# Optimization experiments

Measured on AMD Instinct MI355X. Metric: run time of the kernel, lower is better.

The kernel has to match this reference:

```python
import jax, jax.numpy as jnp
import numpy as np

N_NODES = 50000
N_EDGES = 600000
D_EMB = 128
D_HID = 128
N_HEADS = 4
N_MABS = 7  # ISAB0(mab0,mab1), ISAB1(mab0,mab1), PMA, SAB, SAB
B, S = 16, 512
PROTO = 5


def setup_inputs() -> dict:
    key = jax.random.key(0)
    ks = jax.random.split(key, 24)
    nrm = lambda k, shape, s=0.05: jax.random.normal(k, shape, jnp.float32) * s
    node_embed = nrm(ks[0], (N_NODES + 1, D_EMB), 1.0).at[0].set(0.0)  # padding_idx=0
    return {
        'node_ids': jax.random.randint(ks[1], (B, S), 0, N_NODES),
        'edge_idx': jax.random.randint(ks[2], (2, N_EDGES), 0, N_NODES),
        'edge_attr': jax.random.normal(ks[3], (N_EDGES,), jnp.float32),
        'node_embed': node_embed,
        'lin_W': nrm(ks[4], (D_EMB, D_HID)), 'lin_b': jnp.zeros((D_HID,), jnp.float32),
        'gat_W': nrm(ks[5], (D_HID, D_HID)),
        'gat_att_src': nrm(ks[6], (D_HID,)), 'gat_att_dst': nrm(ks[7], (D_HID,)),
        'gat_bias': jnp.zeros((D_HID,), jnp.float32),
        'mab_Wq': nrm(ks[8], (N_MABS, D_HID, D_HID)), 'mab_bq': jnp.zeros((N_MABS, D_HID), jnp.float32),
        'mab_Wk': nrm(ks[9], (N_MABS, D_HID, D_HID)), 'mab_bk': jnp.zeros((N_MABS, D_HID), jnp.float32),
        'mab_Wv': nrm(ks[10], (N_MABS, D_HID, D_HID)), 'mab_bv': jnp.zeros((N_MABS, D_HID), jnp.float32),
        'mab_Wo': nrm(ks[11], (N_MABS, D_HID, D_HID)), 'mab_bo': jnp.zeros((N_MABS, D_HID), jnp.float32),
        'isab_I': nrm(ks[12], (2, 1, D_HID), 1.0),   # 2 ISAB blocks, num_inds=1
        'pma_S': nrm(ks[13], (1, D_HID), 1.0),       # num_outputs=1 seed
        'dec_W': nrm(ks[14], (D_HID, D_HID)), 'dec_b': jnp.zeros((D_HID,), jnp.float32),
        'prototypes': nrm(ks[15], (1, PROTO, D_HID), 1.0),
    }


def mab(Q, K, Wq, bq, Wk, bk, Wv, bv, Wo, bo):
    # Set-transformer MAB, ln=False; residual uses projected Q; scale by sqrt(full dim)
    D = Q.shape[-1]
    h, d = N_HEADS, D // N_HEADS
    Qp = Q @ Wq + bq
    Kp = K @ Wk + bk
    Vp = K @ Wv + bv
    sh = lambda x: x.reshape(x.shape[0], x.shape[1], h, d).transpose(0, 2, 1, 3)
    A = jax.nn.softmax(jnp.einsum('bhqd,bhkd->bhqk', sh(Qp), sh(Kp)) / np.sqrt(D).astype(np.float32))
    O = sh(Qp) + jnp.einsum('bhqk,bhkd->bhqd', A, sh(Vp))
    O = O.transpose(0, 2, 1, 3).reshape(Q.shape[0], Q.shape[1], D)
    return O + jax.nn.relu(O @ Wo + bo)


def reference(node_ids, edge_idx, edge_attr, node_embed, lin_W, lin_b, gat_W,
              gat_att_src, gat_att_dst, gat_bias, mab_Wq, mab_bq, mab_Wk, mab_bk,
              mab_Wv, mab_bv, mab_Wo, mab_bo, isab_I, pma_S, dec_W, dec_b, prototypes):
    # embed all nodes then linear
    x = node_embed[jnp.arange(N_NODES)] @ lin_W + lin_b          # [N, H]
    # GATConv (1 head, negative_slope=0.2, add_self_loops=True; edge_attr unused)
    loops = jnp.arange(N_NODES)
    src = jnp.concatenate([edge_idx[0], loops])
    dst = jnp.concatenate([edge_idx[1], loops])
    xw = x @ gat_W                                               # [N, H]
    a_s = xw @ gat_att_src                                       # [N]
    a_d = xw @ gat_att_dst
    e = jax.nn.leaky_relu(a_s[src] + a_d[dst], 0.2)              # [E+N]
    m = jax.ops.segment_max(e, dst, num_segments=N_NODES)
    ex = jnp.exp(e - m[dst])
    den = jax.ops.segment_sum(ex, dst, num_segments=N_NODES)
    coef = ex / den[dst]
    x = jax.ops.segment_sum(coef[:, None] * xw[src], dst, num_segments=N_NODES) + gat_bias
    # gather per-sample node sets
    X = x[node_ids]                                              # [B, S, H]
    b = X.shape[0]
    def mb(i, Q, K):
        return mab(Q, K, mab_Wq[i], mab_bq[i], mab_Wk[i], mab_bk[i],
                   mab_Wv[i], mab_bv[i], mab_Wo[i], mab_bo[i])
    # encoder: 2 ISAB blocks (num_inds=1)
    for i in range(2):
        Hb = mb(2 * i, jnp.broadcast_to(isab_I[i][None], (b, 1, D_HID)), X)
        X = mb(2 * i + 1, X, Hb)
    # decoder: PMA -> SAB -> SAB -> Linear
    X = mb(4, jnp.broadcast_to(pma_S[None], (b, 1, D_HID)), X)
    X = mb(5, X, X)
    X = mb(6, X, X)
    X = X @ dec_W + dec_b                                        # [B, 1, H]
    proto = jnp.broadcast_to(prototypes, (b, PROTO, D_HID))
    return jnp.concatenate([X, proto], axis=1)                   # [B, 6, H]
```

## Files before the change

kernel.cpp:

```cpp
#include <hip/hip_runtime.h>
#include <math.h>

#define N_NODES 50000
#define N_EDGES 600000
#define BATCH 16
#define SEQ 512
#define NROWS (BATCH*SEQ)
#define N_ITEMS (N_EDGES + N_NODES)

#define OFF_X      0L
#define OFF_ACC    1048576L
#define OFF_X2     2097152L
#define OFF_WC     3245728L
#define OFF_BC     3262112L
#define OFF_QP     3262240L
#define OFF_WKH    3262624L
#define OFF_CKH    3264160L
#define OFF_VAS    3264176L
#define OFF_VAD    3264304L
#define OFF_BFIN   3264432L
#define OFF_CSD    3264560L
#define OFF_VPOD   3264564L
#define OFF_UP     3266612L
#define OFF_SP     3332148L
#define OFF_PWH    3332660L
#define OFF_PWL    3373620L
#define OFF_MASK   3414580L
#define OFF_DEG    (OFF_MASK + 50000L)
#define OFF_FILL   (OFF_DEG + 8192L)
#define OFF_CNT    (OFF_FILL + 8192L)
#define ZERO_BYTES ((50000L + 8192L + 8192L + 4L) * 4L)
#define OFF_MAP    (OFF_CNT + 4L)
#define OFF_INV    (OFF_MAP + 50000L)
#define OFF_ROWPTR (OFF_INV + 8192L)
#define OFF_COL    (OFF_ROWPTR + 8194L)

typedef __attribute__((ext_vector_type(8))) short bf16x8;
typedef __attribute__((ext_vector_type(4))) float f32x4;
#define MFMA16(a,b,c) __builtin_amdgcn_mfma_f32_16x16x32_bf16(a,b,c,0,0,0)

__device__ __forceinline__ unsigned short f2bf_rne(float f) {
    unsigned int u = __float_as_uint(f);
    unsigned int r = u + 0x7FFFu + ((u >> 16) & 1u);
    return (unsigned short)(r >> 16);
}
__device__ __forceinline__ float bf2f(unsigned short h) {
    return __uint_as_float(((unsigned int)h) << 16);
}
__device__ __forceinline__ float wave_allsum(float x) {
    #pragma unroll
    for (int off = 32; off > 0; off >>= 1) x += __shfl_xor(x, off);
    return x;
}

__global__ __launch_bounds__(256) void prep_kernel(
    const float* __restrict__ lin_W, const float* __restrict__ lin_b,
    const float* __restrict__ gat_W,
    const float* __restrict__ mab_Wq, const float* __restrict__ mab_bq,
    const float* __restrict__ isab_I, const float* __restrict__ pma_S,
    float* __restrict__ Wc, float* __restrict__ bc, float* __restrict__ qp)
{
    int t = blockIdx.x * 256 + threadIdx.x;
    if (t < 16384) {
        int i = t >> 7, j = t & 127;
        float s = 0.f;
        for (int k = 0; k < 128; ++k) s += lin_W[i*128 + k] * gat_W[k*128 + j];
        Wc[t] = s;
    } else if (t < 16512) {
        int j = t - 16384;
        float s = 0.f;
        for (int k = 0; k < 128; ++k) s += lin_b[k] * gat_W[k*128 + j];
        bc[j] = s;
    } else if (t < 16896) {
        int u = t - 16512;
        int m = u >> 7, c = u & 127;
        int mi = m * 2;
        const float* vec = (m == 0) ? isab_I : (m == 1 ? isab_I + 128 : pma_S);
        float s = mab_bq[mi*128 + c];
        for (int k = 0; k < 128; ++k) s += vec[k] * mab_Wq[mi*16384 + k*128 + c];
        qp[u] = s;
    }
}

__global__ __launch_bounds__(256) void pack2_kernel(
    const float* __restrict__ Wc, const float* __restrict__ bc,
    const float* __restrict__ qp,
    const float* __restrict__ mab_Wq, const float* __restrict__ mab_Wo,
    const float* __restrict__ mab_Wk, const float* __restrict__ mab_bk,
    const float* __restrict__ att_src, const float* __restrict__ att_dst,
    const float* __restrict__ gat_bias, const int* __restrict__ node_ids,
    unsigned short* __restrict__ pWh, unsigned short* __restrict__ pWl,
    float* __restrict__ wkh, float* __restrict__ ckh,
    float* __restrict__ vas, float* __restrict__ vad,
    float* __restrict__ bfin, float* __restrict__ csd,
    int* __restrict__ mask)
{
    int b = blockIdx.x, t = threadIdx.x;
    if (b < 320) {
        int tid = b*256 + t;
        int m = tid >> 14;
        int e = tid & 16383;
        int j = e & 7, l = (e>>3) & 63, ct = (e>>9) & 7, kc = e >> 12;
        int k = kc*32 + (l>>4)*8 + j;
        int c = ct*16 + (l & 15);
        const float* src;
        if (m == 0) src = Wc;
        else if (m == 1) src = mab_Wq + 1*16384;
        else if (m == 2) src = mab_Wo + 1*16384;
        else if (m == 3) src = mab_Wq + 3*16384;
        else src = mab_Wo + 3*16384;
        float v = src[k*128 + c];
        unsigned short h = f2bf_rne(v);
        pWh[tid] = h;
        pWl[tid] = f2bf_rne(v - bf2f(h));
    } else if (b == 320) {
        for (int it = 0; it < 6; ++it) {
            int u = it*256 + t;
            int m = u >> 9, h = (u >> 7) & 3, j = u & 127;
            const float* Wk = mab_Wk + (2*m)*16384 + j*128 + h*32;
            const float* q  = qp + m*128 + h*32;
            float s = 0.f;
            #pragma unroll
            for (int d = 0; d < 32; ++d) s += Wk[d] * q[d];
            wkh[u] = s;
        }
        if (t < 12) {
            int m = t >> 2, h = t & 3;
            const float* bk = mab_bk + (2*m)*128 + h*32;
            const float* q  = qp + m*128 + h*32;
            float s = 0.f;
            #pragma unroll
            for (int d = 0; d < 32; ++d) s += bk[d] * q[d];
            ckh[t] = s;
        }
    } else if (b == 321) {
        if (t < 128) {
            float s = 0.f;
            for (int j = 0; j < 128; ++j) s += Wc[t*128 + j] * att_src[j];
            vas[t] = s;
            bfin[t] = bc[t] + gat_bias[t];
        } else {
            int k = t - 128;
            float s = 0.f;
            for (int j = 0; j < 128; ++j) s += Wc[k*128 + j] * att_dst[j];
            vad[k] = s;
        }
        if (t == 0) {
            float s = 0.f;
            for (int j = 0; j < 128; ++j) s += bc[j] * att_src[j];
            csd[0] = s;
        }
        if (t == 1) {
            float s = 0.f;
            for (int j = 0; j < 128; ++j) s += bc[j] * att_dst[j];
            csd[1] = s;
        }
    } else {
        int idx = (b - 322)*256 + t;
        mask[node_ids[idx]] = 1;
    }
}

__device__ __forceinline__ void mfma_stage(
    const float (*Xs)[132], int arow, int ao, int lane,
    const unsigned short* __restrict__ pWh, const unsigned short* __restrict__ pWl,
    f32x4 acc[8])
{
    #pragma unroll
    for (int kc = 0; kc < 4; ++kc) {
        float4 fa = *(const float4*)&Xs[arow][kc*32 + ao];
        float4 fb = *(const float4*)&Xs[arow][kc*32 + ao + 4];
        float f[8] = {fa.x, fa.y, fa.z, fa.w, fb.x, fb.y, fb.z, fb.w};
        bf16x8 ah, al;
        #pragma unroll
        for (int j = 0; j < 8; ++j) {
            unsigned short h = f2bf_rne(f[j]);
            ah[j] = (short)h;
            al[j] = (short)f2bf_rne(f[j] - bf2f(h));
        }
        #pragma unroll
        for (int ct = 0; ct < 8; ++ct) {
            int fo = ((kc*8 + ct)*64 + lane)*8;
            bf16x8 bh = *(const bf16x8*)(pWh + fo);
            bf16x8 bl = *(const bf16x8*)(pWl + fo);
            acc[ct] = MFMA16(ah, bh, acc[ct]);
            acc[ct] = MFMA16(ah, bl, acc[ct]);
            acc[ct] = MFMA16(al, bh, acc[ct]);
        }
    }
}

__device__ __forceinline__ void partA_phase(
    const float (*Xs)[132], const float (*wks)[128], float (*esm)[64],
    const float* __restrict__ ckh, int blk, int t,
    float* __restrict__ up, float* __restrict__ sp)
{
    const float scale = 0.088388347648318447f;
    int wv = t >> 6, lane = t & 63;
    {
        float l = 0.f;
        for (int d4 = 0; d4 < 128; d4 += 4) {
            float4 xv = *(const float4*)&Xs[lane][d4];
            l += xv.x*wks[wv][d4] + xv.y*wks[wv][d4+1]
               + xv.z*wks[wv][d4+2] + xv.w*wks[wv][d4+3];
        }
        float e = __expf((l + ckh[wv]) * scale);
        esm[wv][lane] = e;
        float s = e;
        #pragma unroll
        for (int off = 32; off > 0; off >>= 1) s += __shfl_down(s, off);
        if (lane == 0) sp[blk*4 + wv] = s;
    }
    __syncthreads();
    {
        int hh = t >> 7, d = t & 127;
        float a0 = 0.f, a1 = 0.f;
        for (int k = 0; k < 64; ++k) {
            float xv = Xs[k][d];
            a0 += esm[2*hh][k] * xv;
            a1 += esm[2*hh + 1][k] * xv;
        }
        up[(blk*4 + 2*hh)*128 + d] = a0;
        up[(blk*4 + 2*hh + 1)*128 + d] = a1;
    }
}

__global__ __launch_bounds__(256) void mfma_lin_kernel(
    const float* __restrict__ Xin,
    const unsigned short* __restrict__ pWh, const unsigned short* __restrict__ pWl,
    const float* __restrict__ b1, float* __restrict__ out)
{
    __shared__ float Xs[64][132];
    int t = threadIdx.x;
    long row0 = (long)blockIdx.x * 64;
    #pragma unroll
    for (int i = 0; i < 32; ++i) {
        int idx = i*256 + t;
        int r = idx >> 7, k = idx & 127;
        Xs[r][k] = Xin[(row0 + r)*128 + k];
    }
    __syncthreads();
    int lane = t & 63, wv = t >> 6;
    int arow = wv*16 + (lane & 15), ao = (lane >> 4)*8;
    int crow0 = wv*16 + (lane >> 4)*4, ccol = lane & 15;
    f32x4 acc[8];
    #pragma unroll
    for (int ct = 0; ct < 8; ++ct) { acc[ct][0]=0.f; acc[ct][1]=0.f; acc[ct][2]=0.f; acc[ct][3]=0.f; }
    mfma_stage(Xs, arow, ao, lane, pWh, pWl, acc);
    #pragma unroll
    for (int ct = 0; ct < 8; ++ct) {
        int cc = ct*16 + ccol;
        float bb = b1[cc];
        #pragma unroll
        for (int i = 0; i < 4; ++i)
            out[(row0 + crow0 + i)*128 + cc] = acc[ct][i] + bb;
    }
}

__global__ __launch_bounds__(256) void gatherA_kernel(
    const int* __restrict__ node_ids, const int* __restrict__ map,
    const float* __restrict__ X2, const float* __restrict__ wkh,
    const float* __restrict__ ckh,
    float* __restrict__ X, float* __restrict__ up, float* __restrict__ sp)
{
    __shared__ float Xs[64][132];
    __shared__ float wks[4][128];
    __shared__ float esm[4][64];
    __shared__ int cmap[64];
    int blk = blockIdx.x, t = threadIdx.x;
    long j0 = (long)blk * 64;
    if (t < 64) cmap[t] = map[node_ids[j0 + t]];
    #pragma unroll
    for (int i = 0; i < 2; ++i) { int u = i*256 + t; wks[u >> 7][u & 127] = wkh[u]; }
    __syncthreads();
    #pragma unroll
    for (int i = 0; i < 8; ++i) {
        int idx = i*256 + t;
        int r = idx >> 5, k4 = (idx & 31)*4;
        float4 v = *(const float4*)(X2 + (long)cmap[r]*128 + k4);
        *(float4*)&Xs[r][k4] = v;
        *(float4*)(X + (j0 + r)*128 + k4) = v;
    }
    __syncthreads();
    partA_phase(Xs, wks, esm, ckh, blk, t, up, sp);
}

__global__ __launch_bounds__(256) void odd_fused_kernel(
    const float* __restrict__ Xin,
    const unsigned short* __restrict__ pQh, const unsigned short* __restrict__ pQl,
    const float* __restrict__ bq, const float* __restrict__ vpod,
    const unsigned short* __restrict__ pOh, const unsigned short* __restrict__ pOl,
    const float* __restrict__ bo,
    const float* __restrict__ wkh, const float* __restrict__ ckh,
    float* __restrict__ Xout, float* __restrict__ up, float* __restrict__ sp)
{
    __shared__ float Xs[64][132];
    __shared__ float wks[4][128];
    __shared__ float esm[4][64];
    int blk = blockIdx.x, t = threadIdx.x;
    long row0 = (long)blk * 64;
    #pragma unroll
    for (int i = 0; i < 32; ++i) {
        int idx = i*256 + t;
        int r = idx >> 7, k = idx & 127;
        Xs[r][k] = Xin[(row0 + r)*128 + k];
    }
    #pragma unroll
    for (int i = 0; i < 2; ++i) { int u = i*256 + t; wks[u >> 7][u & 127] = wkh[u]; }
    __syncthreads();
    int lane = t & 63, wv = t >> 6;
    int arow = wv*16 + (lane & 15), ao = (lane >> 4)*8;
    int crow0 = wv*16 + (lane >> 4)*4, ccol = lane & 15;
    int bidx = (int)(row0 >> 9);
    f32x4 acc[8];
    #pragma unroll
    for (int ct = 0; ct < 8; ++ct) { acc[ct][0]=0.f; acc[ct][1]=0.f; acc[ct][2]=0.f; acc[ct][3]=0.f; }
    mfma_stage(Xs, arow, ao, lane, pQh, pQl, acc);
    #pragma unroll
    for (int ct = 0; ct < 8; ++ct) {
        int cc = ct*16 + ccol;
        float bb = bq[cc] + vpod[bidx*128 + cc];
        #pragma unroll
        for (int i = 0; i < 4; ++i) Xs[crow0 + i][cc] = acc[ct][i] + bb;
    }
    #pragma unroll
    for (int ct = 0; ct < 8; ++ct) { acc[ct][0]=0.f; acc[ct][1]=0.f; acc[ct][2]=0.f; acc[ct][3]=0.f; }
    mfma_stage(Xs, arow, ao, lane, pOh, pOl, acc);
    #pragma unroll
    for (int ct = 0; ct < 8; ++ct) {
        int cc = ct*16 + ccol;
        float bb = bo[cc];
        #pragma unroll
        for (int i = 0; i < 4; ++i) {
            float o1 = Xs[crow0 + i][cc];
            float v = o1 + fmaxf(acc[ct][i] + bb, 0.f);
            Xout[(row0 + crow0 + i)*128 + cc] = v;
            Xs[crow0 + i][cc] = v;
        }
    }
    __syncthreads();
    partA_phase(Xs, wks, esm, ckh, blk, t, up, sp);
}

__global__ __launch_bounds__(256) void assign_kernel(
    const int* __restrict__ mask, int* __restrict__ map,
    int* __restrict__ inv, int* __restrict__ counter)
{
    __shared__ int wbase[4];
    int i = blockIdx.x*256 + threadIdx.x;
    bool act = (i < N_NODES) && mask[i];
    unsigned long long m = __ballot(act);
    int lane = threadIdx.x & 63;
    int w = threadIdx.x >> 6;
    if (lane == 0) wbase[w] = __popcll(m);
    __syncthreads();
    if (threadIdx.x == 0) {
        int tot = wbase[0] + wbase[1] + wbase[2] + wbase[3];
        int base = atomicAdd(counter, tot);
        int r = base;
        #pragma unroll
        for (int j = 0; j < 4; ++j) { int cj = wbase[j]; wbase[j] = r; r += cj; }
    }
    __syncthreads();
    if (i < N_NODES) {
        int c = -1;
        if (act) {
            c = wbase[w] + __popcll(m & ((1ull << lane) - 1ull));
            inv[c] = i;
        }
        map[i] = c;
    }
}

__global__ __launch_bounds__(256) void pass1_kernel(
    const int* __restrict__ edge_idx, const int* __restrict__ map,
    int* __restrict__ deg)
{
    int i = blockIdx.x*256 + threadIdx.x;
    if (i >= N_ITEMS) return;
    int dd = (i < N_EDGES) ? edge_idx[N_EDGES + i] : i - N_EDGES;
    int c = map[dd];
    if (c >= 0) atomicAdd(&deg[c], 1);
}

__global__ __launch_bounds__(256) void scan_kernel(const int* __restrict__ deg,
                                                   int* __restrict__ rowptr)
{
    __shared__ int wsum[4];
    int t = threadIdx.x;
    int base = t * 32;
    int s = 0;
    #pragma unroll
    for (int j = 0; j < 32; ++j) s += deg[base + j];
    int lane = t & 63, w = t >> 6;
    int v = s;
    #pragma unroll
    for (int off = 1; off < 64; off <<= 1) {
        int n = __shfl_up(v, off);
        if (lane >= off) v += n;
    }
    if (lane == 63) wsum[w] = v;
    __syncthreads();
    int wo = 0;
    for (int i = 0; i < 4; ++i) if (i < w) wo += wsum[i];
    int run = wo + v - s;
    #pragma unroll
    for (int j = 0; j < 32; ++j) { rowptr[base + j] = run; run += deg[base + j]; }
    if (t == 255) rowptr[8192] = run;
}

__global__ __launch_bounds__(256) void pass2_kernel(
    const int* __restrict__ edge_idx, const int* __restrict__ map,
    const int* __restrict__ rowptr, int* __restrict__ fill,
    int* __restrict__ colx)
{
    int i = blockIdx.x*256 + threadIdx.x;
    if (i >= N_ITEMS) return;
    int s, dd;
    if (i < N_EDGES) { s = edge_idx[i]; dd = edge_idx[N_EDGES + i]; }
    else             { s = dd = i - N_EDGES; }
    int c = map[dd];
    if (c < 0) return;
    int pos = rowptr[c] + atomicAdd(&fill[c], 1);
    colx[pos] = s;
}

__global__ __launch_bounds__(256) void agg_kernel(
    const int* __restrict__ rowptr, const int* __restrict__ colx,
    const int* __restrict__ inv, const int* __restrict__ cnt,
    const float* __restrict__ vas, const float* __restrict__ vad,
    const float* __restrict__ csd,
    const float* __restrict__ embed, float* __restrict__ acc)
{
    int c = blockIdx.x*4 + (threadIdx.x >> 6);
    int lane = threadIdx.x & 63;
    if (c >= *cnt) return;
    float va0 = vas[2*lane], va1 = vas[2*lane + 1];
    float vb0 = vad[2*lane], vb1 = vad[2*lane + 1];
    float csd0 = csd[0], csd1 = csd[1];
    int dd = inv[c];
    float2 wrow = *(const float2*)(embed + (long)dd*128 + lane*2);
    float ad = wave_allsum(wrow.x*vb0 + wrow.y*vb1) + csd1;
    int beg = rowptr[c], end = rowptr[c + 1];
    float s0 = 0.f, s1 = 0.f, den = 0.f;
    for (int j = beg; j < end; ++j) {
        int s = colx[j];
        float2 v = *(const float2*)(embed + (long)s*128 + lane*2);
        float as = wave_allsum(v.x*va0 + v.y*va1) + csd0;
        float e = as + ad;
        e = (e > 0.f) ? e : 0.2f * e;
        float ex = __expf(e);
        den += ex;
        s0 += ex * v.x;
        s1 += ex * v.y;
    }
    float inv_d = 1.f / den;
    float* o = acc + (long)c*128 + lane*2;
    o[0] = s0 * inv_d;
    o[1] = s1 * inv_d;
}

__device__ __forceinline__ float matvec_qs(
    const float* __restrict__ W, const float* xs, float (*red)[128], int t)
{
    int c = t & 127, q = t >> 7;
    float acc = 0.f;
    #pragma unroll
    for (int j = 0; j < 32; ++j) {
        int k = q*32 + j;
        acc += xs[k] * W[k*128 + c];
    }
    red[q][c] = acc;
    __syncthreads();
    float s = 0.f;
    if (t < 128) s = red[0][t] + red[1][t] + red[2][t] + red[3][t];
    __syncthreads();
    return s;
}

__global__ __launch_bounds__(512) void attn_evenB_kernel(
    const float* __restrict__ up, const float* __restrict__ sp,
    const float* __restrict__ qp,
    const float* __restrict__ Wv, const float* __restrict__ bv,
    const float* __restrict__ Wo, const float* __restrict__ bo,
    const float* __restrict__ Wv1, const float* __restrict__ bv1,
    float* __restrict__ vpod)
{
    __shared__ float u_sm[4][128];
    __shared__ float red[4][128];
    __shared__ float qs[128], Ovec[128], Hsm[128];
    int b = blockIdx.x, t = threadIdx.x;
    {
        float s = Wv[t*32] + Wo[t*32] + Wv1[t*32];
        asm volatile("" :: "v"(s));
    }
    if (t < 128) qs[t] = qp[t];
    {
        int h = t >> 7, d = t & 127;
        float s = 0.f, dn = 0.f;
        #pragma unroll
        for (int c = 0; c < 8; ++c) {
            s  += up[((b*8 + c)*4 + h)*128 + d];
            dn += sp[(b*8 + c)*4 + h];
        }
        u_sm[h][d] = s / dn;
    }
    __syncthreads();
    {
        int q4 = t >> 7, c = t & 127, h = c >> 5;
        float a = 0.f;
        #pragma unroll
        for (int j = 0; j < 32; ++j) {
            int k = q4*32 + j;
            a += u_sm[h][k] * Wv[k*128 + c];
        }
        red[q4][c] = a;
    }
    __syncthreads();
    if (t < 128) Ovec[t] = qs[t] + red[0][t] + red[1][t] + red[2][t] + red[3][t] + bv[t];
    __syncthreads();
    float mv = matvec_qs(Wo, Ovec, red, t);
    if (t < 128) Hsm[t] = Ovec[t] + fmaxf(mv + bo[t], 0.f);
    __syncthreads();
    float mv2 = matvec_qs(Wv1, Hsm, red, t);
    if (t < 128) vpod[b*128 + t] = mv2 + bv1[t];
}

__global__ __launch_bounds__(512) void attn_pmaB_kernel(
    const float* __restrict__ up, const float* __restrict__ sp,
    const float* __restrict__ qp,
    const float* __restrict__ mab_Wq, const float* __restrict__ mab_bq,
    const float* __restrict__ mab_Wv, const float* __restrict__ mab_bv,
    const float* __restrict__ mab_Wo, const float* __restrict__ mab_bo,
    const float* __restrict__ dec_W, const float* __restrict__ dec_b,
    const float* __restrict__ protos, float* __restrict__ out)
{
    __shared__ float u_sm[4][128];
    __shared__ float red[4][128];
    __shared__ float qs[128], Ovec[128], S1[128], S2[128];
    int b = blockIdx.x, t = threadIdx.x;
    {
        const float* wq = mab_Wq + 5*16384;
        const float* wv = mab_Wv + 4*16384;
        const float* wo = mab_Wo + 4*16384;
        float s = 0.f;
        #pragma unroll
        for (int i = 0; i < 2; ++i) s += wq[(t + 512*i)*32];
        #pragma unroll
        for (int i = 0; i < 3; ++i) { s += wv[(t + 512*i)*32]; s += wo[(t + 512*i)*32]; }
        s += dec_W[t*32];
        asm volatile("" :: "v"(s));
    }
    if (t < 128) qs[t] = qp[t];
    {
        int h = t >> 7, d = t & 127;
        float s = 0.f, dn = 0.f;
        #pragma unroll
        for (int c = 0; c < 8; ++c) {
            s  += up[((b*8 + c)*4 + h)*128 + d];
            dn += sp[(b*8 + c)*4 + h];
        }
        u_sm[h][d] = s / dn;
    }
    __syncthreads();
    {
        int q4 = t >> 7, c = t & 127, h = c >> 5;
        float a = 0.f;
        #pragma unroll
        for (int j = 0; j < 32; ++j) {
            int k = q4*32 + j;
            a += u_sm[h][k] * (mab_Wv + 4*16384)[k*128 + c];
        }
        red[q4][c] = a;
    }
    __syncthreads();
    if (t < 128) Ovec[t] = qs[t] + red[0][t] + red[1][t] + red[2][t] + red[3][t]
                         + mab_bv[4*128 + t];
    __syncthreads();
    float mv = matvec_qs(mab_Wo + 4*16384, Ovec, red, t);
    if (t < 128) S1[t] = Ovec[t] + fmaxf(mv + mab_bo[4*128 + t], 0.f);
    __syncthreads();
    float q5 = matvec_qs(mab_Wq + 5*16384, S1, red, t);
    float v5 = matvec_qs(mab_Wv + 5*16384, S1, red, t);
    if (t < 128) S2[t] = q5 + mab_bq[5*128 + t] + v5 + mab_bv[5*128 + t];
    __syncthreads();
    float m5 = matvec_qs(mab_Wo + 5*16384, S2, red, t);
    if (t < 128) S1[t] = S2[t] + fmaxf(m5 + mab_bo[5*128 + t], 0.f);
    __syncthreads();
    float q6 = matvec_qs(mab_Wq + 6*16384, S1, red, t);
    float v6 = matvec_qs(mab_Wv + 6*16384, S1, red, t);
    if (t < 128) S2[t] = q6 + mab_bq[6*128 + t] + v6 + mab_bv[6*128 + t];
    __syncthreads();
    float m6 = matvec_qs(mab_Wo + 6*16384, S2, red, t);
    if (t < 128) S1[t] = S2[t] + fmaxf(m6 + mab_bo[6*128 + t], 0.f);
    __syncthreads();
    float y = matvec_qs(dec_W, S1, red, t);
    if (t < 128) out[b*768 + t] = y + dec_b[t];
    {
        int p = t >> 7, c = t & 127;
        out[b*768 + (1 + p)*128 + c] = protos[p*128 + c];
        if (t < 128) out[b*768 + 640 + t] = protos[512 + t];
    }
}

extern "C" void kernel_launch(void* const* d_in, const int* in_sizes, int n_in,
                              void* d_out, int out_size, void* d_ws, size_t ws_size,
                              hipStream_t stream)
{
    (void)in_sizes; (void)n_in; (void)out_size; (void)ws_size;
    const int*   node_ids  = (const int*)d_in[0];
    const int*   edge_idx  = (const int*)d_in[1];
    const float* node_embed= (const float*)d_in[3];
    const float* lin_W     = (const float*)d_in[4];
    const float* lin_b     = (const float*)d_in[5];
    const float* gat_W     = (const float*)d_in[6];
    const float* att_src   = (const float*)d_in[7];
    const float* att_dst   = (const float*)d_in[8];
    const float* gat_bias  = (const float*)d_in[9];
    const float* mab_Wq    = (const float*)d_in[10];
    const float* mab_bq    = (const float*)d_in[11];
    const float* mab_Wk    = (const float*)d_in[12];
    const float* mab_bk    = (const float*)d_in[13];
    const float* mab_Wv    = (const float*)d_in[14];
    const float* mab_bv    = (const float*)d_in[15];
    const float* mab_Wo    = (const float*)d_in[16];
    const float* mab_bo    = (const float*)d_in[17];
    const float* isab_I    = (const float*)d_in[18];
    const float* pma_S     = (const float*)d_in[19];
    const float* dec_W     = (const float*)d_in[20];
    const float* dec_b     = (const float*)d_in[21];
    const float* protos    = (const float*)d_in[22];

    float* ws    = (float*)d_ws;
    float* X     = ws + OFF_X;
    float* acc   = ws + OFF_ACC;
    float* X2    = ws + OFF_X2;
    float* Wc    = ws + OFF_WC;
    float* bc    = ws + OFF_BC;
    float* qp    = ws + OFF_QP;
    float* wkh   = ws + OFF_WKH;
    float* ckh   = ws + OFF_CKH;
    float* vas   = ws + OFF_VAS;
    float* vad   = ws + OFF_VAD;
    float* bfin  = ws + OFF_BFIN;
    float* csd   = ws + OFF_CSD;
    float* vpod  = ws + OFF_VPOD;
    float* up    = ws + OFF_UP;
    float* sp    = ws + OFF_SP;
    unsigned short* pWh = (unsigned short*)(ws + OFF_PWH);
    unsigned short* pWl = (unsigned short*)(ws + OFF_PWL);
    int*   mask  = (int*)(ws + OFF_MASK);
    int*   deg   = (int*)(ws + OFF_DEG);
    int*   fill  = (int*)(ws + OFF_FILL);
    int*   cnt   = (int*)(ws + OFF_CNT);
    int*   map   = (int*)(ws + OFF_MAP);
    int*   inv   = (int*)(ws + OFF_INV);
    int*   rowp  = (int*)(ws + OFF_ROWPTR);
    int*   colx  = (int*)(ws + OFF_COL);
    float* out   = (float*)d_out;

    hipMemsetAsync(ws + OFF_MASK, 0, ZERO_BYTES, stream);

    prep_kernel<<<66, 256, 0, stream>>>(lin_W, lin_b, gat_W, mab_Wq, mab_bq, isab_I, pma_S,
                                        Wc, bc, qp);
    pack2_kernel<<<354, 256, 0, stream>>>(Wc, bc, qp, mab_Wq, mab_Wo, mab_Wk, mab_bk,
                                          att_src, att_dst, gat_bias, node_ids,
                                          pWh, pWl, wkh, ckh, vas, vad, bfin, csd, mask);
    assign_kernel<<<(N_NODES + 255)/256, 256, 0, stream>>>(mask, map, inv, cnt);
    pass1_kernel<<<(N_ITEMS + 255)/256, 256, 0, stream>>>(edge_idx, map, deg);
    scan_kernel<<<1, 256, 0, stream>>>(deg, rowp);
    pass2_kernel<<<(N_ITEMS + 255)/256, 256, 0, stream>>>(edge_idx, map, rowp, fill, colx);
    agg_kernel<<<NROWS/4, 256, 0, stream>>>(rowp, colx, inv, cnt, vas, vad, csd,
                                            node_embed, acc);
    mfma_lin_kernel<<<NROWS/64, 256, 0, stream>>>(acc, pWh, pWl, bfin, X2);
    gatherA_kernel<<<NROWS/64, 256, 0, stream>>>(node_ids, map, X2, wkh, ckh, X, up, sp);

    for (int i = 0; i < 2; ++i) {
        int o = 2*i + 1;
        attn_evenB_kernel<<<16, 512, 0, stream>>>(up, sp, qp + i*128,
                                                  mab_Wv + (2*i)*16384, mab_bv + (2*i)*128,
                                                  mab_Wo + (2*i)*16384, mab_bo + (2*i)*128,
                                                  mab_Wv + o*16384, mab_bv + o*128,
                                                  vpod);
        int mq = 1 + 2*i;
        int mo = 2 + 2*i;
        odd_fused_kernel<<<NROWS/64, 256, 0, stream>>>(X,
                                                       pWh + mq*16384, pWl + mq*16384,
                                                       mab_bq + o*128, vpod,
                                                       pWh + mo*16384, pWl + mo*16384,
                                                       mab_bo + o*128,
                                                       wkh + (i + 1)*512, ckh + (i + 1)*4,
                                                       X, up, sp);
    }
    attn_pmaB_kernel<<<16, 512, 0, stream>>>(up, sp, qp + 256,
                                             mab_Wq, mab_bq, mab_Wv, mab_bv, mab_Wo, mab_bo,
                                             dec_W, dec_b, protos, out);
}
```

Before: 259.9 us.

## Fuse prep kernels and fold even-MAB attention into odd fused kernel

Merges the two weight-preparation kernels into one by computing lin_W·gat_W on the fly and reassociating the attention vectors and bias. It also drops the small per-batch even-MAB attention kernel, so every odd_fused block redundantly recomputes its batch's vector chain of three matvecs. The up/sp buffers are double-buffered to avoid read/write conflicts, and deg/fill zeroing moves into assign_kernel. Tile loads are vectorised to float4. This trades removed kernel launches for redundant per-block matvec work, which is repeated 8 times per batch.

```diff
diff --git a/kernel.cpp b/kernel.cpp
--- a/kernel.cpp
+++ b/kernel.cpp
@@ -11,26 +11,25 @@
 #define OFF_X      0L
 #define OFF_ACC    1048576L
 #define OFF_X2     2097152L
-#define OFF_WC     3245728L
-#define OFF_BC     3262112L
-#define OFF_QP     3262240L
-#define OFF_WKH    3262624L
-#define OFF_CKH    3264160L
-#define OFF_VAS    3264176L
-#define OFF_VAD    3264304L
-#define OFF_BFIN   3264432L
-#define OFF_CSD    3264560L
-#define OFF_VPOD   3264564L
-#define OFF_UP     3266612L
-#define OFF_SP     3332148L
-#define OFF_PWH    3332660L
-#define OFF_PWL    3373620L
-#define OFF_MASK   3414580L
-#define OFF_DEG    (OFF_MASK + 50000L)
+#define OFF_QP     3145728L
+#define OFF_WKH    3146112L
+#define OFF_CKH    3147648L
+#define OFF_VAS    3147664L
+#define OFF_VAD    3147792L
+#define OFF_BFIN   3147920L
+#define OFF_CSD    3148048L
+#define OFF_UPA    3148052L
+#define OFF_SPA    3213588L
+#define OFF_UPB    3214100L
+#define OFF_SPB    3279636L
+#define OFF_PWH    3280148L
+#define OFF_PWL    3321108L
+#define OFF_MASK   3362068L
+#define OFF_CNT    (OFF_MASK + 50000L)
+#define ZERO_BYTES ((50000L + 4L) * 4L)
+#define OFF_DEG    (OFF_CNT + 4L)
 #define OFF_FILL   (OFF_DEG + 8192L)
-#define OFF_CNT    (OFF_FILL + 8192L)
-#define ZERO_BYTES ((50000L + 8192L + 8192L + 4L) * 4L)
-#define OFF_MAP    (OFF_CNT + 4L)
+#define OFF_MAP    (OFF_FILL + 8192L)
 #define OFF_INV    (OFF_MAP + 50000L)
 #define OFF_ROWPTR (OFF_INV + 8192L)
 #define OFF_COL    (OFF_ROWPTR + 8194L)
@@ -53,44 +52,18 @@
     return x;
 }
 
-__global__ __launch_bounds__(256) void prep_kernel(
+__global__ __launch_bounds__(256) void prep_all_kernel(
     const float* __restrict__ lin_W, const float* __restrict__ lin_b,
     const float* __restrict__ gat_W,
     const float* __restrict__ mab_Wq, const float* __restrict__ mab_bq,
+    const float* __restrict__ mab_Wk, const float* __restrict__ mab_bk,
+    const float* __restrict__ mab_Wo,
+    const float* __restrict__ att_src, const float* __restrict__ att_dst,
+    const float* __restrict__ gat_bias,
     const float* __restrict__ isab_I, const float* __restrict__ pma_S,
-    float* __restrict__ Wc, float* __restrict__ bc, float* __restrict__ qp)
-{
-    int t = blockIdx.x * 256 + threadIdx.x;
-    if (t < 16384) {
-        int i = t >> 7, j = t & 127;
-        float s = 0.f;
-        for (int k = 0; k < 128; ++k) s += lin_W[i*128 + k] * gat_W[k*128 + j];
-        Wc[t] = s;
-    } else if (t < 16512) {
-        int j = t - 16384;
-        float s = 0.f;
-        for (int k = 0; k < 128; ++k) s += lin_b[k] * gat_W[k*128 + j];
-        bc[j] = s;
-    } else if (t < 16896) {
-        int u = t - 16512;
-        int m = u >> 7, c = u & 127;
-        int mi = m * 2;
-        const float* vec = (m == 0) ? isab_I : (m == 1 ? isab_I + 128 : pma_S);
-        float s = mab_bq[mi*128 + c];
-        for (int k = 0; k < 128; ++k) s += vec[k] * mab_Wq[mi*16384 + k*128 + c];
-        qp[u] = s;
-    }
-}
-
-__global__ __launch_bounds__(256) void pack2_kernel(
-    const float* __restrict__ Wc, const float* __restrict__ bc,
-    const float* __restrict__ qp,
-    const float* __restrict__ mab_Wq, const float* __restrict__ mab_Wo,
-    const float* __restrict__ mab_Wk, const float* __restrict__ mab_bk,
-    const float* __restrict__ att_src, const float* __restrict__ att_dst,
-    const float* __restrict__ gat_bias, const int* __restrict__ node_ids,
+    const int* __restrict__ node_ids,
     unsigned short* __restrict__ pWh, unsigned short* __restrict__ pWl,
-    float* __restrict__ wkh, float* __restrict__ ckh,
+    float* __restrict__ qp, float* __restrict__ wkh, float* __restrict__ ckh,
     float* __restrict__ vas, float* __restrict__ vad,
     float* __restrict__ bfin, float* __restrict__ csd,
     int* __restrict__ mask)
@@ -103,22 +76,38 @@
         int j = e & 7, l = (e>>3) & 63, ct = (e>>9) & 7, kc = e >> 12;
         int k = kc*32 + (l>>4)*8 + j;
         int c = ct*16 + (l & 15);
-        const float* src;
-        if (m == 0) src = Wc;
-        else if (m == 1) src = mab_Wq + 1*16384;
-        else if (m == 2) src = mab_Wo + 1*16384;
-        else if (m == 3) src = mab_Wq + 3*16384;
-        else src = mab_Wo + 3*16384;
-        float v = src[k*128 + c];
+        float v;
+        if (m == 0) {
+            float s = 0.f;
+            for (int r = 0; r < 128; ++r) s += lin_W[k*128 + r] * gat_W[r*128 + c];
+            v = s;
+        } else {
+            const float* src = (m == 1) ? mab_Wq + 1*16384
+                             : (m == 2) ? mab_Wo + 1*16384
+                             : (m == 3) ? mab_Wq + 3*16384
+                             :            mab_Wo + 3*16384;
+            v = src[k*128 + c];
+        }
         unsigned short h = f2bf_rne(v);
         pWh[tid] = h;
         pWl[tid] = f2bf_rne(v - bf2f(h));
     } else if (b == 320) {
+        __shared__ float qps[384];
+        for (int u = t; u < 384; u += 256) {
+            int m = u >> 7, c = u & 127;
+            int mi = m * 2;
+            const float* vec = (m == 0) ? isab_I : (m == 1 ? isab_I + 128 : pma_S);
+            float s = mab_bq[mi*128 + c];
+            for (int k = 0; k < 128; ++k) s += vec[k] * mab_Wq[mi*16384 + k*128 + c];
+            qps[u] = s;
+            qp[u] = s;
+        }
+        __syncthreads();
         for (int it = 0; it < 6; ++it) {
             int u = it*256 + t;
             int m = u >> 9, h = (u >> 7) & 3, j = u & 127;
             const float* Wk = mab_Wk + (2*m)*16384 + j*128 + h*32;
-            const float* q  = qp + m*128 + h*32;
+            const float* q  = qps + m*128 + h*32;
             float s = 0.f;
             #pragma unroll
             for (int d = 0; d < 32; ++d) s += Wk[d] * q[d];
@@ -127,34 +116,38 @@
         if (t < 12) {
             int m = t >> 2, h = t & 3;
             const float* bk = mab_bk + (2*m)*128 + h*32;
-            const float* q  = qp + m*128 + h*32;
+            const float* q  = qps + m*128 + h*32;
             float s = 0.f;
             #pragma unroll
             for (int d = 0; d < 32; ++d) s += bk[d] * q[d];
             ckh[t] = s;
         }
     } else if (b == 321) {
+        __shared__ float gs[128], gd[128], lb[128];
         if (t < 128) {
-            float s = 0.f;
-            for (int j = 0; j < 128; ++j) s += Wc[t*128 + j] * att_src[j];
+            float s = 0.f, d2 = 0.f;
+            for (int j = 0; j < 128; ++j) {
+                float g = gat_W[t*128 + j];
+                s  += g * att_src[j];
+                d2 += g * att_dst[j];
+            }
+            gs[t] = s; gd[t] = d2; lb[t] = lin_b[t];
+        }
+        __syncthreads();
+        if (t < 128) {
+            float s = 0.f, d2 = 0.f, bcv = 0.f;
+            for (int k = 0; k < 128; ++k) {
+                float lw = lin_W[t*128 + k];
+                s  += lw * gs[k];
+                d2 += lw * gd[k];
+                bcv += lb[k] * gat_W[k*128 + t];
+            }
             vas[t] = s;
-            bfin[t] = bc[t] + gat_bias[t];
-        } else {
-            int k = t - 128;
-            float s = 0.f;
-            for (int j = 0; j < 128; ++j) s += Wc[k*128 + j] * att_dst[j];
-            vad[k] = s;
-        }
-        if (t == 0) {
-            float s = 0.f;
-            for (int j = 0; j < 128; ++j) s += bc[j] * att_src[j];
-            csd[0] = s;
-        }
-        if (t == 1) {
-            float s = 0.f;
-            for (int j = 0; j < 128; ++j) s += bc[j] * att_dst[j];
-            csd[1] = s;
-        }
+            vad[t] = d2;
+            bfin[t] = bcv + gat_bias[t];
+        }
+        if (t == 0) { float s = 0.f; for (int k = 0; k < 128; ++k) s += lb[k]*gs[k]; csd[0] = s; }
+        if (t == 1) { float s = 0.f; for (int k = 0; k < 128; ++k) s += lb[k]*gd[k]; csd[1] = s; }
     } else {
         int idx = (b - 322)*256 + t;
         mask[node_ids[idx]] = 1;
@@ -225,6 +218,24 @@
     }
 }
 
+__device__ __forceinline__ float matvec256(
+    const float* __restrict__ W, const float* xs, float (*red)[128], int t)
+{
+    int c = t & 127, q = t >> 7;
+    float a = 0.f;
+    #pragma unroll
+    for (int j = 0; j < 64; ++j) {
+        int k = q*64 + j;
+        a += xs[k] * W[k*128 + c];
+    }
+    red[q][c] = a;
+    __syncthreads();
+    float s = 0.f;
+    if (t < 128) s = red[0][t] + red[1][t];
+    __syncthreads();
+    return s;
+}
+
 __global__ __launch_bounds__(256) void mfma_lin_kernel(
     const float* __restrict__ Xin,
     const unsigned short* __restrict__ pWh, const unsigned short* __restrict__ pWl,
@@ -234,10 +245,10 @@
     int t = threadIdx.x;
     long row0 = (long)blockIdx.x * 64;
     #pragma unroll
-    for (int i = 0; i < 32; ++i) {
+    for (int i = 0; i < 8; ++i) {
         int idx = i*256 + t;
-        int r = idx >> 7, k = idx & 127;
-        Xs[r][k] = Xin[(row0 + r)*128 + k];
+        int r = idx >> 5, k4 = (idx & 31)*4;
+        *(float4*)&Xs[r][k4] = *(const float4*)(Xin + (row0 + r)*128 + k4);
     }
     __syncthreads();
     int lane = t & 63, wv = t >> 6;
@@ -287,31 +298,73 @@
 
 __global__ __launch_bounds__(256) void odd_fused_kernel(
     const float* __restrict__ Xin,
+    const float* __restrict__ upIn, const float* __restrict__ spIn,
+    const float* __restrict__ qpe,
+    const float* __restrict__ Wv_e, const float* __restrict__ bv_e,
+    const float* __restrict__ Wo_e, const float* __restrict__ bo_e,
     const unsigned short* __restrict__ pQh, const unsigned short* __restrict__ pQl,
-    const float* __restrict__ bq, const float* __restrict__ vpod,
+    const float* __restrict__ bq,
     const unsigned short* __restrict__ pOh, const unsigned short* __restrict__ pOl,
     const float* __restrict__ bo,
+    const float* __restrict__ Wv1, const float* __restrict__ bv1,
     const float* __restrict__ wkh, const float* __restrict__ ckh,
-    float* __restrict__ Xout, float* __restrict__ up, float* __restrict__ sp)
+    float* __restrict__ Xout, float* __restrict__ upOut, float* __restrict__ spOut)
 {
     __shared__ float Xs[64][132];
     __shared__ float wks[4][128];
     __shared__ float esm[4][64];
+    __shared__ float u_sm[4][128];
+    __shared__ float red[2][128];
+    __shared__ float qs[128], Ovec[128], Hsm[128], vp[128];
     int blk = blockIdx.x, t = threadIdx.x;
     long row0 = (long)blk * 64;
-    #pragma unroll
-    for (int i = 0; i < 32; ++i) {
+    int bidx = (int)(row0 >> 9);
+    #pragma unroll
+    for (int i = 0; i < 8; ++i) {
         int idx = i*256 + t;
-        int r = idx >> 7, k = idx & 127;
-        Xs[r][k] = Xin[(row0 + r)*128 + k];
+        int r = idx >> 5, k4 = (idx & 31)*4;
+        *(float4*)&Xs[r][k4] = *(const float4*)(Xin + (row0 + r)*128 + k4);
     }
     #pragma unroll
     for (int i = 0; i < 2; ++i) { int u = i*256 + t; wks[u >> 7][u & 127] = wkh[u]; }
+    if (t < 128) qs[t] = qpe[t];
+    {
+        int d = t & 127;
+        #pragma unroll
+        for (int hh = 0; hh < 2; ++hh) {
+            int h = hh*2 + (t >> 7);
+            float s = 0.f, dn = 0.f;
+            #pragma unroll
+            for (int c = 0; c < 8; ++c) {
+                s  += upIn[((bidx*8 + c)*4 + h)*128 + d];
+                dn += spIn[(bidx*8 + c)*4 + h];
+            }
+            u_sm[h][d] = s / dn;
+        }
+    }
+    __syncthreads();
+    {
+        int q = t >> 7, c = t & 127, h = c >> 5;
+        float a = 0.f;
+        #pragma unroll
+        for (int j = 0; j < 64; ++j) {
+            int k = q*64 + j;
+            a += u_sm[h][k] * Wv_e[k*128 + c];
+        }
+        red[q][c] = a;
+    }
+    __syncthreads();
+    if (t < 128) Ovec[t] = qs[t] + red[0][t] + red[1][t] + bv_e[t];
+    __syncthreads();
+    float mv = matvec256(Wo_e, Ovec, red, t);
+    if (t < 128) Hsm[t] = Ovec[t] + fmaxf(mv + bo_e[t], 0.f);
+    __syncthreads();
+    float mv2 = matvec256(Wv1, Hsm, red, t);
+    if (t < 128) vp[t] = mv2 + bv1[t];
     __syncthreads();
     int lane = t & 63, wv = t >> 6;
     int arow = wv*16 + (lane & 15), ao = (lane >> 4)*8;
     int crow0 = wv*16 + (lane >> 4)*4, ccol = lane & 15;
-    int bidx = (int)(row0 >> 9);
     f32x4 acc[8];
     #pragma unroll
     for (int ct = 0; ct < 8; ++ct) { acc[ct][0]=0.f; acc[ct][1]=0.f; acc[ct][2]=0.f; acc[ct][3]=0.f; }
@@ -319,7 +372,7 @@
     #pragma unroll
     for (int ct = 0; ct < 8; ++ct) {
         int cc = ct*16 + ccol;
-        float bb = bq[cc] + vpod[bidx*128 + cc];
+        float bb = bq[cc] + vp[cc];
         #pragma unroll
         for (int i = 0; i < 4; ++i) Xs[crow0 + i][cc] = acc[ct][i] + bb;
     }
@@ -339,15 +392,17 @@
         }
     }
     __syncthreads();
-    partA_phase(Xs, wks, esm, ckh, blk, t, up, sp);
+    partA_phase(Xs, wks, esm, ckh, blk, t, upOut, spOut);
 }
 
 __global__ __launch_bounds__(256) void assign_kernel(
     const int* __restrict__ mask, int* __restrict__ map,
-    int* __restrict__ inv, int* __restrict__ counter)
+    int* __restrict__ inv, int* __restrict__ counter,
+    int* __restrict__ deg, int* __restrict__ fill)
 {
     __shared__ int wbase[4];
     int i = blockIdx.x*256 + threadIdx.x;
+    if (i < 8192) { deg[i] = 0; fill[i] = 0; }
     bool act = (i < N_NODES) && mask[i];
     unsigned long long m = __ballot(act);
     int lane = threadIdx.x & 63;
@@ -476,54 +531,6 @@
     if (t < 128) s = red[0][t] + red[1][t] + red[2][t] + red[3][t];
     __syncthreads();
     return s;
-}
-
-__global__ __launch_bounds__(512) void attn_evenB_kernel(
-    const float* __restrict__ up, const float* __restrict__ sp,
-    const float* __restrict__ qp,
-    const float* __restrict__ Wv, const float* __restrict__ bv,
-    const float* __restrict__ Wo, const float* __restrict__ bo,
-    const float* __restrict__ Wv1, const float* __restrict__ bv1,
-    float* __restrict__ vpod)
-{
-    __shared__ float u_sm[4][128];
-    __shared__ float red[4][128];
-    __shared__ float qs[128], Ovec[128], Hsm[128];
-    int b = blockIdx.x, t = threadIdx.x;
-    {
-        float s = Wv[t*32] + Wo[t*32] + Wv1[t*32];
-        asm volatile("" :: "v"(s));
-    }
-    if (t < 128) qs[t] = qp[t];
-    {
-        int h = t >> 7, d = t & 127;
-        float s = 0.f, dn = 0.f;
-        #pragma unroll
-        for (int c = 0; c < 8; ++c) {
-            s  += up[((b*8 + c)*4 + h)*128 + d];
-            dn += sp[(b*8 + c)*4 + h];
-        }
-        u_sm[h][d] = s / dn;
-    }
-    __syncthreads();
-    {
-        int q4 = t >> 7, c = t & 127, h = c >> 5;
-        float a = 0.f;
-        #pragma unroll
-        for (int j = 0; j < 32; ++j) {
-            int k = q4*32 + j;
-            a += u_sm[h][k] * Wv[k*128 + c];
-        }
-        red[q4][c] = a;
-    }
-    __syncthreads();
-    if (t < 128) Ovec[t] = qs[t] + red[0][t] + red[1][t] + red[2][t] + red[3][t] + bv[t];
-    __syncthreads();
-    float mv = matvec_qs(Wo, Ovec, red, t);
-    if (t < 128) Hsm[t] = Ovec[t] + fmaxf(mv + bo[t], 0.f);
-    __syncthreads();
-    float mv2 = matvec_qs(Wv1, Hsm, red, t);
-    if (t < 128) vpod[b*128 + t] = mv2 + bv1[t];
 }
 
 __global__ __launch_bounds__(512) void attn_pmaB_kernel(
@@ -635,8 +642,6 @@
     float* X     = ws + OFF_X;
     float* acc   = ws + OFF_ACC;
     float* X2    = ws + OFF_X2;
-    float* Wc    = ws + OFF_WC;
-    float* bc    = ws + OFF_BC;
     float* qp    = ws + OFF_QP;
     float* wkh   = ws + OFF_WKH;
     float* ckh   = ws + OFF_CKH;
@@ -644,15 +649,16 @@
     float* vad   = ws + OFF_VAD;
     float* bfin  = ws + OFF_BFIN;
     float* csd   = ws + OFF_CSD;
-    float* vpod  = ws + OFF_VPOD;
-    float* up    = ws + OFF_UP;
-    float* sp    = ws + OFF_SP;
+    float* upA   = ws + OFF_UPA;
+    float* spA   = ws + OFF_SPA;
+    float* upB   = ws + OFF_UPB;
+    float* spB   = ws + OFF_SPB;
     unsigned short* pWh = (unsigned short*)(ws + OFF_PWH);
     unsigned short* pWl = (unsigned short*)(ws + OFF_PWL);
     int*   mask  = (int*)(ws + OFF_MASK);
+    int*   cnt   = (int*)(ws + OFF_CNT);
     int*   deg   = (int*)(ws + OFF_DEG);
     int*   fill  = (int*)(ws + OFF_FILL);
-    int*   cnt   = (int*)(ws + OFF_CNT);
     int*   map   = (int*)(ws + OFF_MAP);
     int*   inv   = (int*)(ws + OFF_INV);
     int*   rowp  = (int*)(ws + OFF_ROWPTR);
@@ -661,38 +667,35 @@
 
     hipMemsetAsync(ws + OFF_MASK, 0, ZERO_BYTES, stream);
 
-    prep_kernel<<<66, 256, 0, stream>>>(lin_W, lin_b, gat_W, mab_Wq, mab_bq, isab_I, pma_S,
-                                        Wc, bc, qp);
-    pack2_kernel<<<354, 256, 0, stream>>>(Wc, bc, qp, mab_Wq, mab_Wo, mab_Wk, mab_bk,
-                                          att_src, att_dst, gat_bias, node_ids,
-                                          pWh, pWl, wkh, ckh, vas, vad, bfin, csd, mask);
-    assign_kernel<<<(N_NODES + 255)/256, 256, 0, stream>>>(mask, map, inv, cnt);
+    prep_all_kernel<<<354, 256, 0, stream>>>(lin_W, lin_b, gat_W, mab_Wq, mab_bq, mab_Wk,
+                                             mab_bk, mab_Wo, att_src, att_dst, gat_bias,
+                                             isab_I, pma_S, node_ids,
+                                             pWh, pWl, qp, wkh, ckh, vas, vad, bfin, csd, mask);
+    assign_kernel<<<(N_NODES + 255)/256, 256, 0, stream>>>(mask, map, inv, cnt, deg, fill);
     pass1_kernel<<<(N_ITEMS + 255)/256, 256, 0, stream>>>(edge_idx, map, deg);
     scan_kernel<<<1, 256, 0, stream>>>(deg, rowp);
     pass2_kernel<<<(N_ITEMS + 255)/256, 256, 0, stream>>>(edge_idx, map, rowp, fill, colx);
     agg_kernel<<<NROWS/4, 256, 0, stream>>>(rowp, colx, inv, cnt, vas, vad, csd,
                                             node_embed, acc);
     mfma_lin_kernel<<<NROWS/64, 256, 0, stream>>>(acc, pWh, pWl, bfin, X2);
-    gatherA_kernel<<<NROWS/64, 256, 0, stream>>>(node_ids, map, X2, wkh, ckh, X, up, sp);
-
-    for (int i = 0; i < 2; ++i) {
-        int o = 2*i + 1;
-        attn_evenB_kernel<<<16, 512, 0, stream>>>(up, sp, qp + i*128,
-                                                  mab_Wv + (2*i)*16384, mab_bv + (2*i)*128,
-                                                  mab_Wo + (2*i)*16384, mab_bo + (2*i)*128,
-                                                  mab_Wv + o*16384, mab_bv + o*128,
-                                                  vpod);
-        int mq = 1 + 2*i;
-        int mo = 2 + 2*i;
-        odd_fused_kernel<<<NROWS/64, 256, 0, stream>>>(X,
-                                                       pWh + mq*16384, pWl + mq*16384,
-                                                       mab_bq + o*128, vpod,
-                                                       pWh + mo*16384, pWl + mo*16384,
-                                                       mab_bo + o*128,
-                                                       wkh + (i + 1)*512, ckh + (i + 1)*4,
-                                                       X, up, sp);
-    }
-    attn_pmaB_kernel<<<16, 512, 0, stream>>>(up, sp, qp + 256,
+    gatherA_kernel<<<NROWS/64, 256, 0, stream>>>(node_ids, map, X2, wkh, ckh, X, upA, spA);
+
+    odd_fused_kernel<<<NROWS/64, 256, 0, stream>>>(X, upA, spA, qp,
+                                                   mab_Wv, mab_bv, mab_Wo, mab_bo,
+                                                   pWh + 1*16384, pWl + 1*16384, mab_bq + 128,
+                                                   pWh + 2*16384, pWl + 2*16384, mab_bo + 128,
+                                                   mab_Wv + 16384, mab_bv + 128,
+                                                   wkh + 512, ckh + 4,
+                                                   X, upB, spB);
+    odd_fused_kernel<<<NROWS/64, 256, 0, stream>>>(X, upB, spB, qp + 128,
+                                                   mab_Wv + 2*16384, mab_bv + 2*128,
+                                                   mab_Wo + 2*16384, mab_bo + 2*128,
+                                                   pWh + 3*16384, pWl + 3*16384, mab_bq + 3*128,
+                                                   pWh + 4*16384, pWl + 4*16384, mab_bo + 3*128,
+                                                   mab_Wv + 3*16384, mab_bv + 3*128,
+                                                   wkh + 1024, ckh + 8,
+                                                   X, upA, spA);
+    attn_pmaB_kernel<<<16, 512, 0, stream>>>(upA, spA, qp + 256,
                                              mab_Wq, mab_bq, mab_Wv, mab_bv, mab_Wo, mab_bo,
                                              dec_W, dec_b, protos, out);
 }
```

Measured after the change: 258.2 us. No clear change (-0.7%).
